# Optimization experiments

Hardware: AMD Instinct MI355X
Metric: run time of the kernel (lower is better)

## Reference

```python
import jax, jax.numpy as jnp
import numpy as np

B, T = 256, 2048
D = 64           # rnn_embd_dims (== input_dims)
LB = 2           # len(band_names)
DB = D // LB     # band_embedding_dims = 32
L = 2            # rnn_layers
G = 3 * DB       # GRU gate width


def setup_inputs() -> dict:
    key = jax.random.key(0)
    ks = jax.random.split(key, 10)
    s = 0.1
    return {
        "band_ids": jax.random.randint(ks[0], (B, T), 0, LB),
        "dtime": jax.random.uniform(ks[1], (B, T, 1), dtype=jnp.float32),
        "z_last": jax.random.normal(ks[2], (B, D), dtype=jnp.float32),
        # per-band params stacked on a leading band axis
        "proj_W": jax.random.normal(ks[3], (LB, D + 1, DB)) * s,
        "proj_b": jnp.zeros((LB, DB)),
        "Wih": jax.random.normal(ks[4], (LB, L, G, DB)) * s,
        "Whh": jax.random.normal(ks[5], (LB, L, G, DB)) * s,
        "bih": jnp.zeros((LB, L, G)),
        "bhh": jnp.zeros((LB, L, G)),
        "mW1": jax.random.normal(ks[6], (LB, DB, DB)) * s,
        "mb1": jnp.zeros((LB, DB)),
        "mW2": jax.random.normal(ks[7], (LB, DB, 1)) * s,
        "mb2": jnp.zeros((LB, 1)),
    }


def _gru_layer(x, mask, Wih, Whh, bih, bhh):
    # x: [B,T,DB], mask: [B,T] bool (True = valid step; invalid steps keep h)
    gx = jnp.einsum('btd,gd->btg', x, Wih) + bih  # precompute input gates [B,T,3*DB]

    def step(h, inp):
        gx_t, m_t = inp                 # [B,G], [B]
        gh = h @ Whh.T + bhh            # [B,G]
        r = jax.nn.sigmoid(gx_t[:, :DB] + gh[:, :DB])
        z = jax.nn.sigmoid(gx_t[:, DB:2 * DB] + gh[:, DB:2 * DB])
        n = jnp.tanh(gx_t[:, 2 * DB:] + r * gh[:, 2 * DB:])
        hn = (1.0 - z) * n + z * h
        h = jnp.where(m_t[:, None], hn, h)
        return h, h

    h0 = jnp.zeros((x.shape[0], DB), x.dtype)
    _, ys = jax.lax.scan(step, h0, (gx.transpose(1, 0, 2), mask.T))
    return ys.transpose(1, 0, 2)  # [B,T,DB]


def _forward(band_ids, dtime, z_last, proj_W, proj_b, Wih, Whh, bih, bhh, mW1, mb1, mW2, mb2):
    Bn, Tn = band_ids.shape
    outs = []
    for kb in range(LB):
        mask = band_ids == kb  # [B,T]
        # serial_to_parallel: stable-compact valid steps to the front of each row
        order = jnp.argsort(jnp.logical_not(mask), axis=1, stable=True)
        p_mask = jnp.take_along_axis(mask, order, axis=1)
        p_dtime = jnp.take_along_axis(dtime, order[:, :, None], axis=1)
        # dz = z_last tiled over t; gather along t is identity for a t-constant tensor
        p_dz = jnp.broadcast_to(z_last[:, None, :], (Bn, Tn, z_last.shape[-1]))
        x = jnp.concatenate([p_dz, p_dtime], axis=-1) @ proj_W[kb] + proj_b[kb]
        for l in range(L):
            x = _gru_layer(x, p_mask, Wih[kb, l], Whh[kb, l], bih[kb, l], bhh[kb, l])
        # dz_projection MLP: hidden relu layer + linear head -> [B,T,1]
        y = jax.nn.relu(x @ mW1[kb] + mb1[kb]) @ mW2[kb] + mb2[kb]
        outs.append(y)
    return tuple(outs)


def reference(band_ids, dtime, z_last, proj_W, proj_b, Wih, Whh, bih, bhh, mW1, mb1, mW2, mb2):
    return _forward(band_ids, dtime, z_last, proj_W, proj_b, Wih, Whh, bih, bhh, mW1, mb1, mW2, mb2)
```

## Files before the change

kernel.cpp:

```cpp
#include <hip/hip_runtime.h>


typedef float v2f __attribute__((ext_vector_type(2)));

constexpr int Bn  = 256;
constexpr int Tn  = 2048;
constexpr int Dn  = 64;
constexpr int DBn = 32;
constexpr int Ln  = 2;
constexpr int Gn  = 96;
constexpr int Kc  = 32;

#if __has_builtin(__builtin_amdgcn_exp2f)
__device__ __forceinline__ float exp2_fast(float x) { return __builtin_amdgcn_exp2f(x); }
#else
__device__ __forceinline__ float exp2_fast(float x) { return exp2f(x); }
#endif
#if __has_builtin(__builtin_amdgcn_rcpf)
__device__ __forceinline__ float rcp_fast(float x) { return __builtin_amdgcn_rcpf(x); }
#else
__device__ __forceinline__ float rcp_fast(float x) { return 1.0f / x; }
#endif

__device__ __forceinline__ float sigmoid_f(float x) {
  return rcp_fast(1.0f + exp2_fast(-1.4426950408889634f * x));
}
__device__ __forceinline__ float tanh_f(float x) {
  return 1.0f - 2.0f * rcp_fast(1.0f + exp2_fast(2.8853900817779268f * x));
}

template <int CTRL>
__device__ __forceinline__ float dpp_add(float x) {
  int y = __builtin_amdgcn_update_dpp(0, __builtin_bit_cast(int, x), CTRL, 0xf, 0xf, true);
  return x + __builtin_bit_cast(float, y);
}
__device__ __forceinline__ float dppx8_add(float x) { return dpp_add<0x128>(x); }
__device__ __forceinline__ float dpp_row_sum16(float x) {
  x = dpp_add<0x128>(x);
  x = dpp_add<0x124>(x);
  x = dpp_add<0x122>(x);
  x = dpp_add<0x121>(x);
  return x;
}

__device__ __forceinline__ float dot8(const v2f* __restrict__ w, const v2f* __restrict__ h) {
  v2f a = {0.0f, 0.0f};
  #pragma unroll
  for (int q = 0; q < 8; ++q) a = __builtin_elementwise_fma(w[q], h[q], a);
  return a.x + a.y;
}
__device__ __forceinline__ float dot8b(const v2f* __restrict__ w, const v2f* __restrict__ h) {
  v2f a = {0.0f, 0.0f}, b = {0.0f, 0.0f};
  #pragma unroll
  for (int q = 0; q < 4; ++q) {
    a = __builtin_elementwise_fma(w[q], h[q], a);
    b = __builtin_elementwise_fma(w[q + 4], h[q + 4], b);
  }
  a = a + b;
  return a.x + a.y;
}

__device__ __forceinline__ void ld16(const float* p, v2f* d) {
  #pragma unroll
  for (int q = 0; q < 4; ++q) {
    float4 a = ((const float4*)p)[q];
    d[2*q] = (v2f){a.x, a.y}; d[2*q+1] = (v2f){a.z, a.w};
  }
}

__global__ __launch_bounds__(256, 1)
void rnn_decoder(const int* __restrict__ band_ids, const float* __restrict__ dtime,
                 const float* __restrict__ z_last, const float* __restrict__ projW,
                 const float* __restrict__ projB, const float* __restrict__ Wih,
                 const float* __restrict__ Whh, const float* __restrict__ bih,
                 const float* __restrict__ bhh, const float* __restrict__ mW1,
                 const float* __restrict__ mb1, const float* __restrict__ mW2,
                 const float* __restrict__ mb2, float* __restrict__ out) {
  const int b    = blockIdx.x >> 1;
  const int kb   = blockIdx.x & 1;
  const int tid  = threadIdx.x;
  const int w    = tid >> 6;
  const int L    = tid & 63;
  const int e    = (L & 7) | ((L >> 4) << 3);
  const int koff = ((L >> 3) & 1) * 16;

  __shared__ __align__(16) float yd[Tn];
  __shared__ __align__(16) float gxr_[2][Kc][DBn][4];
  __shared__ __align__(16) float h1r_[2][Kc][DBn];
  __shared__ __align__(16) float h2r_[2][Kc][DBn];
  __shared__ __align__(16) float vr_[2][Kc][4];
  __shared__ __align__(16) float xb[DBn], xs[DBn];
  __shared__ int nsh;

  const float mb2v = mb2[kb];

  if (w == 0) {
    {
      const int*   brow = band_ids + b * Tn;
      const float* drow = dtime    + b * Tn;
      int cnt = 0;
      int4 bcache[8];
      #pragma unroll
      for (int it = 0; it < 8; ++it) {
        int4 v = ((const int4*)(brow + L * 32))[it];
        bcache[it] = v;
        cnt += (v.x == kb) + (v.y == kb) + (v.z == kb) + (v.w == kb);
      }
      int incl = cnt;
      #pragma unroll
      for (int dlt = 1; dlt < 64; dlt <<= 1) {
        int v = __shfl_up(incl, dlt, 64);
        if (L >= dlt) incl += v;
      }
      int off = incl - cnt;
      const int n0 = __shfl(incl, 63, 64);
      #pragma unroll
      for (int it = 0; it < 8; ++it) {
        int4   v  = bcache[it];
        float4 dd = ((const float4*)(drow + L * 32))[it];
        if (v.x == kb) yd[off++] = dd.x;
        if (v.y == kb) yd[off++] = dd.y;
        if (v.z == kb) yd[off++] = dd.z;
        if (v.w == kb) yd[off++] = dd.w;
      }
      if (L == 0) nsh = n0;
    }
    {
      const float* pw = projW + (kb * (Dn + 1)) * DBn + e;
      const float* zl = z_last + b * Dn;
      float acc = 0.0f;
      #pragma unroll 8
      for (int k = 0; k < Dn; ++k) acc = fmaf(zl[k], pw[k * DBn], acc);
      xb[e] = acc + projB[kb * DBn + e];
      xs[e] = pw[Dn * DBn];
    }
    __builtin_amdgcn_wave_barrier();
    const float* wih1  = Wih + ((kb * Ln + 0) * Gn) * DBn;
    const float* bih1p = bih + (kb * Ln + 0) * Gn;
    const float* bhh1p = bhh + (kb * Ln + 0) * Gn;
    float gb_r = 0, gb_z = 0, gb_n = 0, gs_r = 0, gs_z = 0, gs_n = 0;
    #pragma unroll 4
    for (int j = 0; j < DBn; ++j) {
      float xbv = xb[j], xsv = xs[j];
      float wr = wih1[(     e) * DBn + j];
      float wz = wih1[(32 + e) * DBn + j];
      float wn = wih1[(64 + e) * DBn + j];
      gb_r = fmaf(wr, xbv, gb_r);  gs_r = fmaf(wr, xsv, gs_r);
      gb_z = fmaf(wz, xbv, gb_z);  gs_z = fmaf(wz, xsv, gs_z);
      gb_n = fmaf(wn, xbv, gb_n);  gs_n = fmaf(wn, xsv, gs_n);
    }
    gb_r += bih1p[e]      + bhh1p[e];
    gb_z += bih1p[32 + e] + bhh1p[32 + e];
    gb_n += bih1p[64 + e];
    const float bhh1n = bhh1p[64 + e];
    v2f w1r[8], w1z[8], w1n[8];
    const float* whh1 = Whh + ((kb * Ln + 0) * Gn) * DBn;
    ld16(whh1 + (     e) * DBn + koff, w1r);
    ld16(whh1 + (32 + e) * DBn + koff, w1z);
    ld16(whh1 + (64 + e) * DBn + koff, w1n);
    __syncthreads();

#if __has_builtin(__builtin_amdgcn_s_setprio)
    __builtin_amdgcn_s_setprio(1);
#endif
    const int n = nsh;
    const int C = (n + Kc - 1) >> 5;
    v2f h1a[8];
    #pragma unroll
    for (int q = 0; q < 8; ++q) h1a[q] = (v2f){0.0f, 0.0f};
    float h1self = 0.0f;
    for (int c = 0; c < C + 4; ++c) {
      if (c < C) {
        float* ring = &h1r_[c & 1][0][0];
        const int t0 = c * Kc;
        for (int k = 0; k < Kc; ++k) {
          float d  = yd[t0 + k];
          float ar = dot8b(w1r, h1a);
          float az = dot8b(w1z, h1a);
          float an = dot8b(w1n, h1a);
          ar = dppx8_add(ar);
          az = dppx8_add(az);
          an = dppx8_add(an);
          float r1 = sigmoid_f(fmaf(d, gs_r, gb_r) + ar);
          float z1 = sigmoid_f(fmaf(d, gs_z, gb_z) + az);
          float n1 = tanh_f(fmaf(d, gs_n, gb_n) + r1 * (an + bhh1n));
          h1self = fmaf(z1, h1self - n1, n1);
          ring[k * DBn + e] = h1self;
          __builtin_amdgcn_wave_barrier();
          ld16(&ring[k * DBn + koff], h1a);
        }
      }
      __syncthreads();
    }
  } else if (w == 1) {
    const float* wih2 = Wih + ((kb * Ln + 1) * Gn) * DBn;
    v2f wa[8], wbv[8], wcv[8];
    ld16(wih2 + (     e) * DBn + koff, wa);
    ld16(wih2 + (32 + e) * DBn + koff, wbv);
    ld16(wih2 + (64 + e) * DBn + koff, wcv);
    __syncthreads();

    const int n = nsh;
    const int C = (n + Kc - 1) >> 5;
    for (int c = 0; c < C + 4; ++c) {
      if (c >= 1 && c <= C) {
        const int cp = c - 1;
        const float* hsrc = &h1r_[cp & 1][0][0];
        for (int k = 0; k < Kc; ++k) {
          v2f hb[8];
          ld16(&hsrc[k * DBn + koff], hb);
          float g0 = dot8(wa,  hb);
          float g1 = dot8(wbv, hb);
          float g2 = dot8(wcv, hb);
          g0 = dppx8_add(g0);
          g1 = dppx8_add(g1);
          g2 = dppx8_add(g2);
          float4 gv; gv.x = g0; gv.y = g1; gv.z = g2; gv.w = 0.0f;
          *(float4*)&gxr_[cp & 1][k][e][0] = gv;
        }
      }
      if (c >= 4) {
        const int cd = c - 4;
        if (cd < C && L < 32) {
          float4 p = *(const float4*)&vr_[cd & 1][L][0];
          yd[cd * Kc + L] = ((p.x + p.y) + (p.z + p.w)) + mb2v;
        }
      }
      __syncthreads();
    }
  } else if (w == 2) {
    const float* whh2  = Whh + ((kb * Ln + 1) * Gn) * DBn;
    const float* bih2p = bih + (kb * Ln + 1) * Gn;
    const float* bhh2p = bhh + (kb * Ln + 1) * Gn;
    v2f r2w[8], z2w[8], n2w[8];
    ld16(whh2 + (     e) * DBn + koff, r2w);
    ld16(whh2 + (32 + e) * DBn + koff, z2w);
    ld16(whh2 + (64 + e) * DBn + koff, n2w);
    const float c2r   = bih2p[e]      + bhh2p[e];
    const float c2z   = bih2p[32 + e] + bhh2p[32 + e];
    const float bih2n = bih2p[64 + e];
    const float bhh2n = bhh2p[64 + e];
    __syncthreads();

#if __has_builtin(__builtin_amdgcn_s_setprio)
    __builtin_amdgcn_s_setprio(1);
#endif
    const int n = nsh;
    const int C = (n + Kc - 1) >> 5;
    v2f h2a[8];
    #pragma unroll
    for (int q = 0; q < 8; ++q) h2a[q] = (v2f){0.0f, 0.0f};
    float h2self = 0.0f;
    for (int c = 0; c < C + 4; ++c) {
      if (c >= 2 && c <= C + 1) {
        const int cc = c - 2;
        float* ring = &h2r_[cc & 1][0][0];
        for (int k = 0; k < Kc; ++k) {
          float4 g = *(const float4*)&gxr_[cc & 1][k][e][0];
          float cr = dot8b(r2w, h2a);
          float cz = dot8b(z2w, h2a);
          float cn = dot8b(n2w, h2a);
          cr = dppx8_add(cr);
          cz = dppx8_add(cz);
          cn = dppx8_add(cn);
          float r2v = sigmoid_f(g.x + cr + c2r);
          float z2v = sigmoid_f(g.y + cz + c2z);
          float n2v = tanh_f(g.z + bih2n + r2v * (cn + bhh2n));
          h2self = fmaf(z2v, h2self - n2v, n2v);
          ring[k * DBn + e] = h2self;
          __builtin_amdgcn_wave_barrier();
          ld16(&ring[k * DBn + koff], h2a);
        }
      }
      __syncthreads();
    }
  } else {
    v2f m1c[8];
    #pragma unroll
    for (int q = 0; q < 8; ++q)
      m1c[q] = (v2f){ mW1[(kb * DBn + koff + 2*q)     * DBn + e],
                      mW1[(kb * DBn + koff + 2*q + 1) * DBn + e] };
    const float mb1e = mb1[kb * DBn + e];
    const float mW2h = 0.5f * mW2[kb * DBn + e];
    {
      float p = fmaxf(mb1e, 0.0f) * mW2h;
      p = dpp_row_sum16(p);
      if ((L & 15) == 15) vr_[0][L >> 4][(L >> 4) & 3] = p;
    }
    {
      float p = fmaxf(mb1e, 0.0f) * mW2h;
      p = dpp_row_sum16(p);
      if ((L & 15) == 15) vr_[0][0][L >> 4] = p;
    }
    __syncthreads();

    const int n = nsh;
    const int C = (n + Kc - 1) >> 5;
    for (int c = 0; c < C + 4; ++c) {
      if (c >= 3 && c <= C + 2) {
        const int cm = c - 3;
        const float* hsrc = &h2r_[cm & 1][0][0];
        for (int k = 0; k < Kc; ++k) {
          v2f hb[8];
          ld16(&hsrc[k * DBn + koff], hb);
          float mh = dot8(m1c, hb);
          mh = dppx8_add(mh);
          float v = fmaxf(mh + mb1e, 0.0f) * mW2h;
          v = dpp_row_sum16(v);
          if ((L & 15) == 15) vr_[cm & 1][k][L >> 4] = v;
        }
      }
      __syncthreads();
    }
  }

  const int n = nsh;
  float ylast;
  if (n > 0) {
    ylast = yd[n - 1];
  } else {
    float4 p = *(const float4*)&vr_[0][0][0];
    ylast = ((p.x + p.y) + (p.z + p.w)) + mb2v;
  }
  for (int t = n + tid; t < Tn; t += 256) yd[t] = ylast;
  __syncthreads();

  float* orow = out + (kb * Bn + b) * Tn;
  for (int q = tid; q < Tn / 4; q += 256)
    ((float4*)orow)[q] = ((const float4*)yd)[q];
}

extern "C" void kernel_launch(void* const* d_in, const int* in_sizes, int n_in,
                              void* d_out, int out_size, void* d_ws, size_t ws_size,
                              hipStream_t stream) {
  const int*   band_ids = (const int*)  d_in[0];
  const float* dtime    = (const float*)d_in[1];
  const float* z_last   = (const float*)d_in[2];
  const float* projW    = (const float*)d_in[3];
  const float* projB    = (const float*)d_in[4];
  const float* Wih      = (const float*)d_in[5];
  const float* Whh      = (const float*)d_in[6];
  const float* bihp     = (const float*)d_in[7];
  const float* bhhp     = (const float*)d_in[8];
  const float* mW1      = (const float*)d_in[9];
  const float* mb1      = (const float*)d_in[10];
  const float* mW2      = (const float*)d_in[11];
  const float* mb2      = (const float*)d_in[12];
  float* out = (float*)d_out;
  rnn_decoder<<<dim3(Bn * 2), dim3(256), 0, stream>>>(
      band_ids, dtime, z_last, projW, projB, Wih, Whh, bihp, bhhp,
      mW1, mb1, mW2, mb2, out);
}
```

Measured before the change: 323.4 us.

## Merge four-wave pipeline into two waves by fusing layer-2 input gates and MLP

```diff
diff --git a/kernel.cpp b/kernel.cpp
--- a/kernel.cpp
+++ b/kernel.cpp
@@ -68,7 +68,7 @@
   }
 }
 
-__global__ __launch_bounds__(256, 1)
+__global__ __launch_bounds__(128, 1)
 void rnn_decoder(const int* __restrict__ band_ids, const float* __restrict__ dtime,
                  const float* __restrict__ z_last, const float* __restrict__ projW,
                  const float* __restrict__ projB, const float* __restrict__ Wih,
@@ -86,9 +86,9 @@
 
   __shared__ __align__(16) float yd[Tn];
   __shared__ __align__(16) float gxr_[2][Kc][DBn][4];
-  __shared__ __align__(16) float h1r_[2][Kc][DBn];
-  __shared__ __align__(16) float h2r_[2][Kc][DBn];
   __shared__ __align__(16) float vr_[2][Kc][4];
+  __shared__ __align__(16) float h1b[DBn];
+  __shared__ __align__(16) float h2b[DBn];
   __shared__ __align__(16) float xb[DBn], xs[DBn];
   __shared__ int nsh;
 
@@ -158,26 +158,37 @@
     ld16(whh1 + (     e) * DBn + koff, w1r);
     ld16(whh1 + (32 + e) * DBn + koff, w1z);
     ld16(whh1 + (64 + e) * DBn + koff, w1n);
+    v2f wa[8], wbv[8], wcv[8];
+    const float* wih2 = Wih + ((kb * Ln + 1) * Gn) * DBn;
+    ld16(wih2 + (     e) * DBn + koff, wa);
+    ld16(wih2 + (32 + e) * DBn + koff, wbv);
+    ld16(wih2 + (64 + e) * DBn + koff, wcv);
     __syncthreads();
 
-#if __has_builtin(__builtin_amdgcn_s_setprio)
-    __builtin_amdgcn_s_setprio(1);
-#endif
     const int n = nsh;
     const int C = (n + Kc - 1) >> 5;
     v2f h1a[8];
     #pragma unroll
     for (int q = 0; q < 8; ++q) h1a[q] = (v2f){0.0f, 0.0f};
     float h1self = 0.0f;
-    for (int c = 0; c < C + 4; ++c) {
+    for (int c = 0; c < C + 2; ++c) {
       if (c < C) {
-        float* ring = &h1r_[c & 1][0][0];
+        float* gxc = &gxr_[c & 1][0][0][0];
         const int t0 = c * Kc;
         for (int k = 0; k < Kc; ++k) {
           float d  = yd[t0 + k];
           float ar = dot8b(w1r, h1a);
           float az = dot8b(w1z, h1a);
           float an = dot8b(w1n, h1a);
+          float g0 = dot8(wa,  h1a);
+          float g1 = dot8(wbv, h1a);
+          float g2 = dot8(wcv, h1a);
+          g0 = dppx8_add(g0);
+          g1 = dppx8_add(g1);
+          g2 = dppx8_add(g2);
+          const int kw = k - (k > 0);
+          float4 gv; gv.x = g0; gv.y = g1; gv.z = g2; gv.w = 0.0f;
+          *(float4*)&gxc[(kw * DBn + e) * 4] = gv;
           ar = dppx8_add(ar);
           az = dppx8_add(az);
           an = dppx8_add(an);
@@ -185,50 +196,24 @@
           float z1 = sigmoid_f(fmaf(d, gs_z, gb_z) + az);
           float n1 = tanh_f(fmaf(d, gs_n, gb_n) + r1 * (an + bhh1n));
           h1self = fmaf(z1, h1self - n1, n1);
-          ring[k * DBn + e] = h1self;
+          h1b[e] = h1self;
           __builtin_amdgcn_wave_barrier();
-          ld16(&ring[k * DBn + koff], h1a);
+          ld16(&h1b[koff], h1a);
         }
-      }
-      __syncthreads();
-    }
-  } else if (w == 1) {
-    const float* wih2 = Wih + ((kb * Ln + 1) * Gn) * DBn;
-    v2f wa[8], wbv[8], wcv[8];
-    ld16(wih2 + (     e) * DBn + koff, wa);
-    ld16(wih2 + (32 + e) * DBn + koff, wbv);
-    ld16(wih2 + (64 + e) * DBn + koff, wcv);
-    __syncthreads();
-
-    const int n = nsh;
-    const int C = (n + Kc - 1) >> 5;
-    for (int c = 0; c < C + 4; ++c) {
-      if (c >= 1 && c <= C) {
-        const int cp = c - 1;
-        const float* hsrc = &h1r_[cp & 1][0][0];
-        for (int k = 0; k < Kc; ++k) {
-          v2f hb[8];
-          ld16(&hsrc[k * DBn + koff], hb);
-          float g0 = dot8(wa,  hb);
-          float g1 = dot8(wbv, hb);
-          float g2 = dot8(wcv, hb);
+        {
+          float g0 = dot8(wa,  h1a);
+          float g1 = dot8(wbv, h1a);
+          float g2 = dot8(wcv, h1a);
           g0 = dppx8_add(g0);
           g1 = dppx8_add(g1);
           g2 = dppx8_add(g2);
           float4 gv; gv.x = g0; gv.y = g1; gv.z = g2; gv.w = 0.0f;
-          *(float4*)&gxr_[cp & 1][k][e][0] = gv;
+          *(float4*)&gxc[((Kc - 1) * DBn + e) * 4] = gv;
         }
       }
-      if (c >= 4) {
-        const int cd = c - 4;
-        if (cd < C && L < 32) {
-          float4 p = *(const float4*)&vr_[cd & 1][L][0];
-          yd[cd * Kc + L] = ((p.x + p.y) + (p.z + p.w)) + mb2v;
-        }
-      }
       __syncthreads();
     }
-  } else if (w == 2) {
+  } else {
     const float* whh2  = Whh + ((kb * Ln + 1) * Gn) * DBn;
     const float* bih2p = bih + (kb * Ln + 1) * Gn;
     const float* bhh2p = bhh + (kb * Ln + 1) * Gn;
@@ -240,41 +225,6 @@
     const float c2z   = bih2p[32 + e] + bhh2p[32 + e];
     const float bih2n = bih2p[64 + e];
     const float bhh2n = bhh2p[64 + e];
-    __syncthreads();
-
-#if __has_builtin(__builtin_amdgcn_s_setprio)
-    __builtin_amdgcn_s_setprio(1);
-#endif
-    const int n = nsh;
-    const int C = (n + Kc - 1) >> 5;
-    v2f h2a[8];
-    #pragma unroll
-    for (int q = 0; q < 8; ++q) h2a[q] = (v2f){0.0f, 0.0f};
-    float h2self = 0.0f;
-    for (int c = 0; c < C + 4; ++c) {
-      if (c >= 2 && c <= C + 1) {
-        const int cc = c - 2;
-        float* ring = &h2r_[cc & 1][0][0];
-        for (int k = 0; k < Kc; ++k) {
-          float4 g = *(const float4*)&gxr_[cc & 1][k][e][0];
-          float cr = dot8b(r2w, h2a);
-          float cz = dot8b(z2w, h2a);
-          float cn = dot8b(n2w, h2a);
-          cr = dppx8_add(cr);
-          cz = dppx8_add(cz);
-          cn = dppx8_add(cn);
-          float r2v = sigmoid_f(g.x + cr + c2r);
-          float z2v = sigmoid_f(g.y + cz + c2z);
-          float n2v = tanh_f(g.z + bih2n + r2v * (cn + bhh2n));
-          h2self = fmaf(z2v, h2self - n2v, n2v);
-          ring[k * DBn + e] = h2self;
-          __builtin_amdgcn_wave_barrier();
-          ld16(&ring[k * DBn + koff], h2a);
-        }
-      }
-      __syncthreads();
-    }
-  } else {
     v2f m1c[8];
     #pragma unroll
     for (int q = 0; q < 8; ++q)
@@ -285,48 +235,73 @@
     {
       float p = fmaxf(mb1e, 0.0f) * mW2h;
       p = dpp_row_sum16(p);
-      if ((L & 15) == 15) vr_[0][L >> 4][(L >> 4) & 3] = p;
-    }
-    {
-      float p = fmaxf(mb1e, 0.0f) * mW2h;
-      p = dpp_row_sum16(p);
       if ((L & 15) == 15) vr_[0][0][L >> 4] = p;
     }
     __syncthreads();
 
     const int n = nsh;
     const int C = (n + Kc - 1) >> 5;
-    for (int c = 0; c < C + 4; ++c) {
-      if (c >= 3 && c <= C + 2) {
-        const int cm = c - 3;
-        const float* hsrc = &h2r_[cm & 1][0][0];
+    v2f h2a[8];
+    #pragma unroll
+    for (int q = 0; q < 8; ++q) h2a[q] = (v2f){0.0f, 0.0f};
+    float h2self = 0.0f;
+    for (int c = 0; c < C + 2; ++c) {
+      if (c >= 1 && c <= C) {
+        const int cc = c - 1;
+        const float* gxc = &gxr_[cc & 1][0][0][0];
+        float* vrc = &vr_[cc & 1][0][0];
         for (int k = 0; k < Kc; ++k) {
-          v2f hb[8];
-          ld16(&hsrc[k * DBn + koff], hb);
-          float mh = dot8(m1c, hb);
+          float4 g = *(const float4*)&gxc[(k * DBn + e) * 4];
+          float cr = dot8b(r2w, h2a);
+          float cz = dot8b(z2w, h2a);
+          float cn = dot8b(n2w, h2a);
+          float mh = dot8(m1c, h2a);
           mh = dppx8_add(mh);
           float v = fmaxf(mh + mb1e, 0.0f) * mW2h;
           v = dpp_row_sum16(v);
-          if ((L & 15) == 15) vr_[cm & 1][k][L >> 4] = v;
+          const int kw = k - (k > 0);
+          if ((L & 15) == 15) vrc[kw * 4 + (L >> 4)] = v;
+          cr = dppx8_add(cr);
+          cz = dppx8_add(cz);
+          cn = dppx8_add(cn);
+          float r2v = sigmoid_f(g.x + cr + c2r);
+          float z2v = sigmoid_f(g.y + cz + c2z);
+          float n2v = tanh_f(g.z + bih2n + r2v * (cn + bhh2n));
+          h2self = fmaf(z2v, h2self - n2v, n2v);
+          h2b[e] = h2self;
+          __builtin_amdgcn_wave_barrier();
+          ld16(&h2b[koff], h2a);
         }
+        {
+          float mh = dot8(m1c, h2a);
+          mh = dppx8_add(mh);
+          float v = fmaxf(mh + mb1e, 0.0f) * mW2h;
+          v = dpp_row_sum16(v);
+          if ((L & 15) == 15) vrc[(Kc - 1) * 4 + (L >> 4)] = v;
+        }
+      }
+      if (c >= 2 && L < 32) {
+        const int cd = c - 2;
+        float4 p = *(const float4*)&vr_[cd & 1][L][0];
+        yd[cd * Kc + L] = ((p.x + p.y) + (p.z + p.w)) + mb2v;
       }
       __syncthreads();
     }
   }
 
-  const int n = nsh;
+  const int nf = nsh;
   float ylast;
-  if (n > 0) {
-    ylast = yd[n - 1];
+  if (nf > 0) {
+    ylast = yd[nf - 1];
   } else {
     float4 p = *(const float4*)&vr_[0][0][0];
     ylast = ((p.x + p.y) + (p.z + p.w)) + mb2v;
   }
-  for (int t = n + tid; t < Tn; t += 256) yd[t] = ylast;
+  for (int t = nf + tid; t < Tn; t += 128) yd[t] = ylast;
   __syncthreads();
 
   float* orow = out + (kb * Bn + b) * Tn;
-  for (int q = tid; q < Tn / 4; q += 256)
+  for (int q = tid; q < Tn / 4; q += 128)
     ((float4*)orow)[q] = ((const float4*)yd)[q];
 }
 
@@ -347,7 +322,7 @@
   const float* mW2      = (const float*)d_in[11];
   const float* mb2      = (const float*)d_in[12];
   float* out = (float*)d_out;
-  rnn_decoder<<<dim3(Bn * 2), dim3(256), 0, stream>>>(
+  rnn_decoder<<<dim3(Bn * 2), dim3(128), 0, stream>>>(
       band_ids, dtime, z_last, projW, projB, Wih, Whh, bihp, bhhp,
       mW1, mb1, mW2, mb2, out);
 }
```

New measurement: 495.6 us. 53.3% more time.
